# Kernel optimization log

Measured on AMD Instinct MI355X. Metric: run time of the kernel, lower is better.

## Reference

```python
import jax, jax.numpy as jnp
import numpy as np

WINDOW = 21
PATCH = 1
H_PARAM = 0.1
EPS = 1e-10


def _box_sum(x, w):
    # Sum over a w x w sliding window (VALID), per (batch, channel).
    return jax.lax.reduce_window(x, 0.0, jax.lax.add,
                                 (1, 1, w, w), (1, 1, 1, 1), 'VALID')


def setup_inputs() -> dict:
    key = jax.random.key(0)
    noisy = jax.random.uniform(key, (8, 3, 512, 512), dtype=jnp.float32)
    return {"noisy": noisy}


def reference(noisy) -> jnp.ndarray:
    # Faithful vectorization of the per-pixel loop for patch_size=1.
    # For each pixel p=(i,j):
    #   window = padded[i:i+W, j:j+W]; center = noisy[i,j]
    #   dists  = mean((window - center)^2)
    #   weights = exp(-dists / h^2)            # shape (B, C)
    #   patch  = window[0, 0] = padded[i, j]   # top-left of window (half_patch=0)
    #   out[:, c, i, j] = sum_b weights[b,c] * patch[b,c]   (sum over BATCH)
    #   wsum[:, c, i, j] = sum_b weights[b,c]
    # out = clamp(out / (wsum + 1e-10), 0, 1)
    h2 = H_PARAM * H_PARAM
    W = WINDOW
    pad = W // 2
    B, C, Hh, Ww = noisy.shape
    padded = jnp.pad(noisy, ((0, 0), (0, 0), (pad, pad), (pad, pad)), mode='reflect')

    # mean((window - center)^2) = (S2 - 2*center*S1 + W^2*center^2) / W^2
    s1 = _box_sum(padded, W)                  # (B, C, H, W)
    s2 = _box_sum(padded * padded, W)
    n_win = jnp.asarray(W * W, dtype=noisy.dtype)
    dists = (s2 - 2.0 * noisy * s1 + n_win * noisy * noisy) / n_win

    weights = jnp.exp(-dists / h2)            # (B, C, H, W)
    patch = padded[:, :, :Hh, :Ww]            # top-left pixel of each window

    num = jnp.sum(weights * patch, axis=0, keepdims=True)   # (1, C, H, W)
    den = jnp.sum(weights, axis=0, keepdims=True)
    out = num / (den + EPS)
    out = jnp.broadcast_to(out, noisy.shape)  # loop assigns same row to all b
    return jnp.clip(out, 0.0, 1.0)
```

## Files before the change

### kernel.cpp

```cpp
#include <hip/hip_runtime.h>

#define B 8
#define CCH 3
#define HH 512
#define WW 512
#define PAD 10
#define TSX 32
#define TSY 32
#define PTY 52
#define TROW 60
#define HSH 53
#define NSLOT 676
#define NT 128
#define NPRE 6

__global__ __launch_bounds__(NT) void nlm_fused_kernel(const float* __restrict__ noisy,
                                                       float* __restrict__ out) {
    __shared__ float  tile[PTY][TROW];
    __shared__ float2 hs_t[TSX][HSH];

    const int tid = threadIdx.x;
    const int x0 = blockIdx.x * TSX;
    const int y0 = blockIdx.y * TSY;
    const int ch = blockIdx.z;

    int   rowbase[NPRE], gxs[NPRE];
    float* ldsp[NPRE];
    bool  valid[NPRE], edge[NPRE];
    #pragma unroll
    for (int k = 0; k < NPRE; ++k) {
        int s = tid + NT * k;
        valid[k] = (s < NSLOT);
        int ss = valid[k] ? s : 0;
        int r  = ss / 13;
        int c4 = ss - r * 13;
        int gy = y0 + r - PAD;
        gy = (gy < 0) ? -gy : ((gy >= HH) ? (2 * (HH - 1) - gy) : gy);
        int gx = x0 + (c4 << 2) - PAD;
        rowbase[k] = gy * WW;
        gxs[k]     = gx;
        edge[k]    = (gx < 0) || (gx > WW - 4);
        ldsp[k]    = &tile[r][c4 << 2];
    }

    float4 pre[NPRE];
    auto prefetch = [&](int bb) {
        const float* src = noisy + (size_t)(bb * CCH + ch) * (HH * WW);
        #pragma unroll
        for (int k = 0; k < NPRE; ++k) {
            if (valid[k]) {
                if (!edge[k]) {
                    pre[k] = *(const float4*)(src + rowbase[k] + gxs[k]);
                } else {
                    float tmp[4];
                    #pragma unroll
                    for (int t = 0; t < 4; ++t) {
                        int gx = gxs[k] + t;
                        gx = (gx < 0) ? -gx : ((gx >= WW) ? (2 * (WW - 1) - gx) : gx);
                        tmp[t] = src[rowbase[k] + gx];
                    }
                    pre[k] = make_float4(tmp[0], tmp[1], tmp[2], tmp[3]);
                }
            }
        }
    };

    const int tx  = tid & 31;
    const int ty0 = (tid >> 5) << 3;
    const int x   = x0 + tx;
    int px = x - PAD;  px = (px < 0) ? -px : px;
    const int a_base = (y0 + ty0) * WW + x;
    int p_off[8];
    #pragma unroll
    for (int i = 0; i < 8; ++i) {
        int py = y0 + ty0 + i - PAD;
        py = (py < 0) ? -py : py;
        p_off[i] = py * WW + px;
    }

    const int hrow = tid >> 1;
    const int hseg = (tid & 1) << 4;

    float num[8], den[8];
    #pragma unroll
    for (int i = 0; i < 8; ++i) { num[i] = 0.f; den[i] = 0.f; }

    prefetch(0);

    for (int b = 0; b < B; ++b) {
        const float* src = noisy + (size_t)(b * CCH + ch) * (HH * WW);
        __syncthreads();
        #pragma unroll
        for (int k = 0; k < NPRE; ++k)
            if (valid[k]) *(float4*)ldsp[k] = pre[k];
        __syncthreads();

        if (b < B - 1) prefetch(b + 1);

        float av[8], pv[8];
        #pragma unroll
        for (int i = 0; i < 8; ++i) {
            av[i] = src[a_base + i * WW];
            pv[i] = src[p_off[i]];
        }

        if (tid < PTY * 2) {
            float v[36];
            #pragma unroll
            for (int q = 0; q < 9; ++q)
                *(float4*)&v[q * 4] = *(const float4*)&tile[hrow][hseg + (q << 2)];
            float s1 = 0.f, s2 = 0.f;
            #pragma unroll
            for (int k = 0; k <= 20; ++k) { s1 += v[k]; s2 = fmaf(v[k], v[k], s2); }
            hs_t[hseg][hrow] = make_float2(s1, s2);
            #pragma unroll
            for (int j = 1; j < 16; ++j) {
                float vo = v[j - 1], vn = v[j + 20];
                s1 += vn - vo;
                s2 += vn * vn - vo * vo;
                hs_t[hseg + j][hrow] = make_float2(s1, s2);
            }
        }
        __syncthreads();

        float2 hh[21];
        #pragma unroll
        for (int k = 0; k < 21; ++k) hh[k] = hs_t[tx][ty0 + k];
        float vs1 = 0.f, vs2 = 0.f;
        #pragma unroll
        for (int k = 0; k < 21; ++k) { vs1 += hh[k].x; vs2 += hh[k].y; }

        const float kE = (-100.0f / 441.0f) * 1.44269504088896f;
        {
            float a = av[0];
            float dd = fmaf(a, fmaf(441.f, a, -2.f * vs1), vs2);
            float w = exp2f(dd * kE);
            num[0] += w * pv[0]; den[0] += w;
        }
        #pragma unroll
        for (int i = 1; i < 8; ++i) {
            float2 hn = hs_t[tx][ty0 + 20 + i];
            vs1 += hn.x - hh[i - 1].x;
            vs2 += hn.y - hh[i - 1].y;
            float a = av[i];
            float dd = fmaf(a, fmaf(441.f, a, -2.f * vs1), vs2);
            float w = exp2f(dd * kE);
            num[i] += w * pv[i]; den[i] += w;
        }
    }

    #pragma unroll
    for (int i = 0; i < 8; ++i) {
        int y = y0 + ty0 + i;
        float v = num[i] / (den[i] + 1e-10f);
        v = v < 0.f ? 0.f : (v > 1.f ? 1.f : v);
        #pragma unroll
        for (int b = 0; b < B; ++b)
            out[((size_t)(b * CCH + ch) * HH + y) * WW + x] = v;
    }
}

extern "C" void kernel_launch(void* const* d_in, const int* in_sizes, int n_in,
                              void* d_out, int out_size, void* d_ws, size_t ws_size,
                              hipStream_t stream) {
    const float* noisy = (const float*)d_in[0];
    float* out = (float*)d_out;
    dim3 grid(WW / TSX, HH / TSY, CCH);
    nlm_fused_kernel<<<grid, dim3(NT), 0, stream>>>(noisy, out);
}
```

Measured before the change: 90.02 us.

## Split block into producer and consumer warps with double-buffered horizontal sums

Doubles the block to 256 threads. The first 128 threads load rows straight from global memory and compute horizontal box sums into a double-buffered LDS array for the next batch image. The other 128 threads do the vertical sums, exponentials and accumulation for the current image, so the raw-tile LDS staging and one barrier per iteration are removed. The cost is twice the threads per block, idle producer lanes beyond row 52, unaligned float4 global loads, and doubled LDS for the hs buffer.

```diff
diff --git a/kernel.cpp b/kernel.cpp
--- a/kernel.cpp
+++ b/kernel.cpp
@@ -8,155 +8,143 @@
 #define TSX 32
 #define TSY 32
 #define PTY 52
-#define TROW 60
 #define HSH 53
-#define NSLOT 676
-#define NT 128
-#define NPRE 6
+#define NT 256
 
-__global__ __launch_bounds__(NT) void nlm_fused_kernel(const float* __restrict__ noisy,
-                                                       float* __restrict__ out) {
-    __shared__ float  tile[PTY][TROW];
-    __shared__ float2 hs_t[TSX][HSH];
+__global__ __launch_bounds__(NT, 3) void nlm_fused_kernel(const float* __restrict__ noisy,
+                                                          float* __restrict__ out) {
+    __shared__ float2 hs[2][TSX][HSH];
 
     const int tid = threadIdx.x;
     const int x0 = blockIdx.x * TSX;
     const int y0 = blockIdx.y * TSY;
     const int ch = blockIdx.z;
+    const bool is_prod = (tid < 128);
 
-    int   rowbase[NPRE], gxs[NPRE];
-    float* ldsp[NPRE];
-    bool  valid[NPRE], edge[NPRE];
-    #pragma unroll
-    for (int k = 0; k < NPRE; ++k) {
-        int s = tid + NT * k;
-        valid[k] = (s < NSLOT);
-        int ss = valid[k] ? s : 0;
-        int r  = ss / 13;
-        int c4 = ss - r * 13;
-        int gy = y0 + r - PAD;
+    const float kE = (-100.0f / 441.0f) * 1.44269504088896f;
+
+    const bool pact = is_prod && (tid < PTY * 2);
+    const int  prow = tid >> 1;
+    const int  pseg = (tid & 1) << 4;
+    int prowbase = 0, pgx0 = 0;
+    bool pedge = false;
+    if (is_prod) {
+        int gy = y0 + prow - PAD;
         gy = (gy < 0) ? -gy : ((gy >= HH) ? (2 * (HH - 1) - gy) : gy);
-        int gx = x0 + (c4 << 2) - PAD;
-        rowbase[k] = gy * WW;
-        gxs[k]     = gx;
-        edge[k]    = (gx < 0) || (gx > WW - 4);
-        ldsp[k]    = &tile[r][c4 << 2];
+        prowbase = gy * WW;
+        pgx0 = x0 + pseg - 12;
+        pedge = (pgx0 < 0) || (pgx0 + 39 > WW - 1);
     }
 
-    float4 pre[NPRE];
-    auto prefetch = [&](int bb) {
+    auto hsum = [&](int bb, int buf) {
         const float* src = noisy + (size_t)(bb * CCH + ch) * (HH * WW);
+        float v[40];
+        if (!pedge) {
+            #pragma unroll
+            for (int q = 0; q < 10; ++q)
+                *(float4*)&v[q * 4] = *(const float4*)(src + prowbase + pgx0 + (q << 2));
+        } else {
+            #pragma unroll
+            for (int t = 0; t < 40; ++t) {
+                int gx = pgx0 + t;
+                gx = (gx < 0) ? -gx : ((gx >= WW) ? (2 * (WW - 1) - gx) : gx);
+                v[t] = src[prowbase + gx];
+            }
+        }
+        float s1 = 0.f, s2 = 0.f;
         #pragma unroll
-        for (int k = 0; k < NPRE; ++k) {
-            if (valid[k]) {
-                if (!edge[k]) {
-                    pre[k] = *(const float4*)(src + rowbase[k] + gxs[k]);
-                } else {
-                    float tmp[4];
-                    #pragma unroll
-                    for (int t = 0; t < 4; ++t) {
-                        int gx = gxs[k] + t;
-                        gx = (gx < 0) ? -gx : ((gx >= WW) ? (2 * (WW - 1) - gx) : gx);
-                        tmp[t] = src[rowbase[k] + gx];
-                    }
-                    pre[k] = make_float4(tmp[0], tmp[1], tmp[2], tmp[3]);
-                }
-            }
+        for (int k = 2; k <= 22; ++k) { s1 += v[k]; s2 = fmaf(v[k], v[k], s2); }
+        if (pact) hs[buf][pseg][prow] = make_float2(s1, s2);
+        #pragma unroll
+        for (int j = 1; j < 16; ++j) {
+            float vo = v[j + 1], vn = v[j + 22];
+            s1 += vn - vo;
+            s2 += vn * vn - vo * vo;
+            if (pact) hs[buf][pseg + j][prow] = make_float2(s1, s2);
         }
     };
 
-    const int tx  = tid & 31;
-    const int ty0 = (tid >> 5) << 3;
-    const int x   = x0 + tx;
-    int px = x - PAD;  px = (px < 0) ? -px : px;
-    const int a_base = (y0 + ty0) * WW + x;
-    int p_off[8];
+    const int ctid = tid - 128;
+    const int tx   = ctid & 31;
+    const int cty0 = (ctid >> 5) << 3;
+    const int x    = x0 + tx;
+    int px = x - PAD; px = (px < 0) ? -px : px;
+    const int abase = (y0 + cty0) * WW + x;
+    int poff[8];
     #pragma unroll
     for (int i = 0; i < 8; ++i) {
-        int py = y0 + ty0 + i - PAD;
+        int py = y0 + cty0 + i - PAD;
         py = (py < 0) ? -py : py;
-        p_off[i] = py * WW + px;
+        poff[i] = py * WW + px;
     }
 
-    const int hrow = tid >> 1;
-    const int hseg = (tid & 1) << 4;
+    float avp[8], pvp[8];
+    auto ap_prefetch = [&](int bb) {
+        const float* src = noisy + (size_t)(bb * CCH + ch) * (HH * WW);
+        #pragma unroll
+        for (int i = 0; i < 8; ++i) {
+            avp[i] = src[abase + i * WW];
+            pvp[i] = src[poff[i]];
+        }
+    };
 
     float num[8], den[8];
     #pragma unroll
     for (int i = 0; i < 8; ++i) { num[i] = 0.f; den[i] = 0.f; }
 
-    prefetch(0);
+    if (is_prod) {
+        hsum(0, 0);
+    } else {
+        ap_prefetch(0);
+    }
+    __syncthreads();
 
     for (int b = 0; b < B; ++b) {
-        const float* src = noisy + (size_t)(b * CCH + ch) * (HH * WW);
-        __syncthreads();
-        #pragma unroll
-        for (int k = 0; k < NPRE; ++k)
-            if (valid[k]) *(float4*)ldsp[k] = pre[k];
-        __syncthreads();
+        if (is_prod) {
+            if (b < B - 1) hsum(b + 1, (b + 1) & 1);
+        } else {
+            const int cur = b & 1;
+            float av[8], pv[8];
+            #pragma unroll
+            for (int i = 0; i < 8; ++i) { av[i] = avp[i]; pv[i] = pvp[i]; }
+            if (b < B - 1) ap_prefetch(b + 1);
 
-        if (b < B - 1) prefetch(b + 1);
-
-        float av[8], pv[8];
-        #pragma unroll
-        for (int i = 0; i < 8; ++i) {
-            av[i] = src[a_base + i * WW];
-            pv[i] = src[p_off[i]];
-        }
-
-        if (tid < PTY * 2) {
-            float v[36];
+            float2 hh[21];
             #pragma unroll
-            for (int q = 0; q < 9; ++q)
-                *(float4*)&v[q * 4] = *(const float4*)&tile[hrow][hseg + (q << 2)];
-            float s1 = 0.f, s2 = 0.f;
+            for (int k = 0; k < 21; ++k) hh[k] = hs[cur][tx][cty0 + k];
+            float vs1 = 0.f, vs2 = 0.f;
             #pragma unroll
-            for (int k = 0; k <= 20; ++k) { s1 += v[k]; s2 = fmaf(v[k], v[k], s2); }
-            hs_t[hseg][hrow] = make_float2(s1, s2);
+            for (int k = 0; k < 21; ++k) { vs1 += hh[k].x; vs2 += hh[k].y; }
+            {
+                float a = av[0];
+                float dd = fmaf(a, fmaf(441.f, a, -2.f * vs1), vs2);
+                float w = exp2f(dd * kE);
+                num[0] += w * pv[0]; den[0] += w;
+            }
             #pragma unroll
-            for (int j = 1; j < 16; ++j) {
-                float vo = v[j - 1], vn = v[j + 20];
-                s1 += vn - vo;
-                s2 += vn * vn - vo * vo;
-                hs_t[hseg + j][hrow] = make_float2(s1, s2);
+            for (int i = 1; i < 8; ++i) {
+                float2 hn = hs[cur][tx][cty0 + 20 + i];
+                vs1 += hn.x - hh[i - 1].x;
+                vs2 += hn.y - hh[i - 1].y;
+                float a = av[i];
+                float dd = fmaf(a, fmaf(441.f, a, -2.f * vs1), vs2);
+                float w = exp2f(dd * kE);
+                num[i] += w * pv[i]; den[i] += w;
             }
         }
         __syncthreads();
-
-        float2 hh[21];
-        #pragma unroll
-        for (int k = 0; k < 21; ++k) hh[k] = hs_t[tx][ty0 + k];
-        float vs1 = 0.f, vs2 = 0.f;
-        #pragma unroll
-        for (int k = 0; k < 21; ++k) { vs1 += hh[k].x; vs2 += hh[k].y; }
-
-        const float kE = (-100.0f / 441.0f) * 1.44269504088896f;
-        {
-            float a = av[0];
-            float dd = fmaf(a, fmaf(441.f, a, -2.f * vs1), vs2);
-            float w = exp2f(dd * kE);
-            num[0] += w * pv[0]; den[0] += w;
-        }
-        #pragma unroll
-        for (int i = 1; i < 8; ++i) {
-            float2 hn = hs_t[tx][ty0 + 20 + i];
-            vs1 += hn.x - hh[i - 1].x;
-            vs2 += hn.y - hh[i - 1].y;
-            float a = av[i];
-            float dd = fmaf(a, fmaf(441.f, a, -2.f * vs1), vs2);
-            float w = exp2f(dd * kE);
-            num[i] += w * pv[i]; den[i] += w;
-        }
     }
 
-    #pragma unroll
-    for (int i = 0; i < 8; ++i) {
-        int y = y0 + ty0 + i;
-        float v = num[i] / (den[i] + 1e-10f);
-        v = v < 0.f ? 0.f : (v > 1.f ? 1.f : v);
+    if (!is_prod) {
         #pragma unroll
-        for (int b = 0; b < B; ++b)
-            out[((size_t)(b * CCH + ch) * HH + y) * WW + x] = v;
+        for (int i = 0; i < 8; ++i) {
+            int y = y0 + cty0 + i;
+            float v = num[i] / (den[i] + 1e-10f);
+            v = v < 0.f ? 0.f : (v > 1.f ? 1.f : v);
+            #pragma unroll
+            for (int b = 0; b < B; ++b)
+                out[((size_t)(b * CCH + ch) * HH + y) * WW + x] = v;
+        }
     }
 }
 
```

Result: slower. 154.4 us (+71.6%).
